# Performance work log

Measured on AMD Instinct MI355X. Metric: run time of the kernel, lower is better.

## Reference

```python
import jax, jax.numpy as jnp
import numpy as np

# Level-7 icosphere: nv vertices, nf faces
NV, NF = 163842, 327680
IN_C, NECK_C, OUT_C, B = 64, 32, 128, 2
EPS = 1e-5


def setup_inputs() -> dict:
    key = jax.random.key(0)
    ks = jax.random.split(key, 16)
    f32 = jnp.float32
    d = {}
    d['x'] = jax.random.normal(ks[0], (B, IN_C, NV), f32)
    # conv1 (1x1), bn1
    d['w1'] = jax.random.normal(ks[1], (NECK_C, IN_C), f32) * 0.05
    d['b1'] = jnp.zeros((NECK_C,), f32)
    d['gamma1'] = jnp.ones((NECK_C,), f32); d['beta1'] = jnp.zeros((NECK_C,), f32)
    # MeshConv: coeffs (out,in,4 taps: id, lap, grad_ew, grad_ns) + bias
    d['coeffs'] = jax.random.normal(ks[2], (NECK_C, NECK_C, 4), f32) * 0.05
    d['mc_bias'] = jnp.zeros((NECK_C,), f32)
    d['gamma2'] = jnp.ones((NECK_C,), f32); d['beta2'] = jnp.zeros((NECK_C,), f32)
    # conv3 (1x1), bn3
    d['w3'] = jax.random.normal(ks[3], (OUT_C, NECK_C), f32) * 0.05
    d['b3'] = jnp.zeros((OUT_C,), f32)
    d['gamma3'] = jnp.ones((OUT_C,), f32); d['beta3'] = jnp.zeros((OUT_C,), f32)
    # shortcut conv_ + bn_ (diff_chan since in!=out)
    d['wsc'] = jax.random.normal(ks[4], (OUT_C, IN_C), f32) * 0.05
    d['bsc'] = jnp.zeros((OUT_C,), f32)
    d['gammasc'] = jnp.ones((OUT_C,), f32); d['betasc'] = jnp.zeros((OUT_C,), f32)
    # sparse mesh operators (gather indices + values):
    # G: face gradient, 3 components per face from 3 face vertices
    d['idx_G'] = jax.random.randint(ks[5], (NF, 3), 0, NV, jnp.int32)
    d['vals_G'] = jax.random.normal(ks[6], (NF, 3, 3), f32) * 0.1
    # EW/NS tangent direction per face (3-vectors)
    d['EW'] = jax.random.normal(ks[7], (NF, 3), f32)
    d['NS'] = jax.random.normal(ks[8], (NF, 3), f32)
    # L: vertex laplacian, ~7 nnz per row
    d['idx_L'] = jax.random.randint(ks[9], (NV, 7), 0, NV, jnp.int32)
    d['vals_L'] = jax.random.normal(ks[10], (NV, 7), f32) * 0.1
    # F2V: face-to-vertex averaging, ~6 faces per vertex
    d['idx_F2V'] = jax.random.randint(ks[11], (NV, 6), 0, NF, jnp.int32)
    d['vals_F2V'] = jax.random.uniform(ks[12], (NV, 6), f32) / 6.0
    return d


def _bn(x, g, b):
    # training-mode BatchNorm1d over (batch, spatial), per channel
    m = x.mean(axis=(0, 2), keepdims=True)
    v = ((x - m) ** 2).mean(axis=(0, 2), keepdims=True)
    return g[None, :, None] * (x - m) * jax.lax.rsqrt(v + EPS) + b[None, :, None]


def _conv1x1(x, w, b):
    return jnp.einsum('oc,bcn->bon', w, x) + b[None, :, None]


def _mesh_conv(x, coeffs, bias, idx_G, vals_G, EW, NS, idx_L, vals_L, idx_F2V, vals_F2V):
    # laplacian: sparse matmul via gather  (B,C,NV)
    lap = jnp.einsum('bcnk,nk->bcn', x[:, :, idx_L], vals_L)
    # face gradient: (B,C,NF,3 components)
    grad_face = jnp.einsum('bcfj,fij->bcfi', x[:, :, idx_G], vals_G)
    g_ew = jnp.einsum('bcfi,fi->bcf', grad_face, EW)
    g_ns = jnp.einsum('bcfi,fi->bcf', grad_face, NS)
    # face -> vertex averaging
    gv_ew = jnp.einsum('bcnk,nk->bcn', g_ew[:, :, idx_F2V], vals_F2V)
    gv_ns = jnp.einsum('bcnk,nk->bcn', g_ns[:, :, idx_F2V], vals_F2V)
    feat = jnp.stack([x, lap, gv_ew, gv_ns], axis=-1)  # (B,C,NV,4)
    return jnp.einsum('bcnk,ock->bon', feat, coeffs) + bias[None, :, None]


def reference(x, w1, b1, gamma1, beta1, coeffs, mc_bias, gamma2, beta2,
              w3, b3, gamma3, beta3, wsc, bsc, gammasc, betasc,
              idx_G, vals_G, EW, NS, idx_L, vals_L, idx_F2V, vals_F2V):
    # shortcut branch (diff_chan)
    x2 = _bn(_conv1x1(x, wsc, bsc), gammasc, betasc)
    # main branch
    h = jax.nn.relu(_bn(_conv1x1(x, w1, b1), gamma1, beta1))
    h = _mesh_conv(h, coeffs, mc_bias, idx_G, vals_G, EW, NS, idx_L, vals_L, idx_F2V, vals_F2V)
    h = jax.nn.relu(_bn(h, gamma2, beta2))
    h = _bn(_conv1x1(h, w3, b3), gamma3, beta3)
    return jax.nn.relu(h + x2)
```

## Files before the change

### kernel.cpp

```cpp
#include <hip/hip_runtime.h>

#define NV   163842
#define NF   327680
#define BB   2
#define INC  64
#define NECK 32
#define OUTC 128
#define NT   (BB*NV)
#define EPSB 1e-5f

typedef unsigned short ushort_t;
typedef __attribute__((ext_vector_type(8))) short bf16x8;
typedef __attribute__((ext_vector_type(4))) float f32x4;

#define F_SX8  0
#define F_SS8  512
#define F_A1   33280
#define F_C1   33312
#define F_ASC  33344
#define F_CSC  33472
#define F_S2S  33600
#define F_S2Q  33632
#define F_A2   33664
#define F_C2   33696
#define F_SHR  33728
#define F_SS2  33760
#define F_A3   34784
#define F_C3   34912
#define F_CF   35040
#define STATN  35168
#define F_W1B  35200
#define F_CFB  36224
#define F_Y1   38272
#define F_H2   (F_Y1 + NT*16)
#define F_I18  (F_H2 + NT*16)
#define F_WEW  (F_I18 + NV*18)
#define F_WNS  (F_WEW + NV*18)
#define F_XB   (F_WNS + NV*18)

#define FSTR 136

__device__ __forceinline__ float bf2f(ushort_t u) {
    union { unsigned int i; float f; } x; x.i = ((unsigned int)u) << 16; return x.f;
}
__device__ __forceinline__ ushort_t f2bf(float f) {
    union { float f; unsigned int i; } x; x.f = f;
    unsigned int r = x.i + 0x7fffu + ((x.i >> 16) & 1u);
    return (ushort_t)(r >> 16);
}

__global__ __launch_bounds__(256) void k_xcvt(const float* __restrict__ x,
                                              float* __restrict__ ws,
                                              ushort_t* __restrict__ xb) {
    __shared__ float SSl[64 * 68 + 64];
    const int tid = threadIdx.x;
    const int w = tid >> 6, l = tid & 63;
    const int o16 = l & 15, kg = l >> 4;

    for (int i = tid; i < 64 * 68 + 64; i += 256) SSl[i] = 0.f;
    __syncthreads();

    f32x4 acc[10];
#pragma unroll
    for (int i = 0; i < 10; ++i) acc[i] = (f32x4){0.f, 0.f, 0.f, 0.f};
    f32x4 accS[4];
#pragma unroll
    for (int i = 0; i < 4; ++i) accS[i] = (f32x4){0.f, 0.f, 0.f, 0.f};

    bf16x8 onesf;
    {
        short ov = (o16 == 0) ? (short)0x3F80 : (short)0;
#pragma unroll
        for (int j = 0; j < 8; ++j) onesf[j] = ov;
    }

    const int NCHB = (NV + 63) >> 6;
    const int NW = gridDim.x * 4;
    for (int cid = blockIdx.x * 4 + w; cid < 2 * NCHB; cid += NW) {
        const int b = (cid >= NCHB) ? 1 : 0;
        const int tc = cid - b * NCHB;
        const int n0 = tc << 6;
        const float* xsrc = x + (size_t)b * 64 * NV;
        const bool full = (n0 + 64 <= NV);
        const int n = n0 + l;
        if (n < NV) {
            unsigned int pk[32];
#pragma unroll
            for (int c2 = 0; c2 < 32; ++c2) {
                float f0 = xsrc[(size_t)(2 * c2) * NV + n];
                float f1 = xsrc[(size_t)(2 * c2 + 1) * NV + n];
                pk[c2] = (unsigned int)f2bf(f0) | ((unsigned int)f2bf(f1) << 16);
            }
            ushort_t* row = xb + (size_t)(b * NV + n) * 64;
#pragma unroll
            for (int j = 0; j < 8; ++j) {
                uint4 q = make_uint4(pk[4 * j], pk[4 * j + 1], pk[4 * j + 2], pk[4 * j + 3]);
                *(uint4*)(row + j * 8) = q;
            }
        }
        bf16x8 fr[4][2];
#pragma unroll
        for (int mt = 0; mt < 4; ++mt) {
            const float* rp = xsrc + (size_t)(mt * 16 + o16) * NV + n0;
#pragma unroll
            for (int ks = 0; ks < 2; ++ks) {
                const int v0 = ks * 32 + kg * 8;
                float f[8];
                if (full) {
                    float4 q0 = *(const float4*)(rp + v0);
                    float4 q1 = *(const float4*)(rp + v0 + 4);
                    f[0] = q0.x; f[1] = q0.y; f[2] = q0.z; f[3] = q0.w;
                    f[4] = q1.x; f[5] = q1.y; f[6] = q1.z; f[7] = q1.w;
                } else {
#pragma unroll
                    for (int j = 0; j < 8; ++j)
                        f[j] = (n0 + v0 + j < NV) ? rp[v0 + j] : 0.f;
                }
                bf16x8 fb;
#pragma unroll
                for (int j = 0; j < 8; ++j) fb[j] = (short)f2bf(f[j]);
                fr[mt][ks] = fb;
            }
        }
#pragma unroll
        for (int ks = 0; ks < 2; ++ks) {
            int tt = 0;
#pragma unroll
            for (int mt = 0; mt < 4; ++mt) {
#pragma unroll
                for (int nt2 = 0; nt2 < 4; ++nt2) {
                    if (nt2 >= mt) {
                        acc[tt] = __builtin_amdgcn_mfma_f32_16x16x32_bf16(fr[mt][ks], fr[nt2][ks], acc[tt], 0, 0, 0);
                        ++tt;
                    }
                }
                accS[mt] = __builtin_amdgcn_mfma_f32_16x16x32_bf16(onesf, fr[mt][ks], accS[mt], 0, 0, 0);
            }
        }
    }
    {
        int tt = 0;
#pragma unroll
        for (int mt = 0; mt < 4; ++mt) {
#pragma unroll
            for (int nt2 = 0; nt2 < 4; ++nt2) {
                if (nt2 >= mt) {
#pragma unroll
                    for (int r = 0; r < 4; ++r) {
                        const int row = mt * 16 + kg * 4 + r;
                        const int col = nt2 * 16 + o16;
                        atomicAdd(&SSl[row * 68 + col], acc[tt][r]);
                    }
                    ++tt;
                }
            }
            if (kg == 0) atomicAdd(&SSl[64 * 68 + mt * 16 + o16], accS[mt][0]);
        }
    }
    __syncthreads();
    {
        float* SSg = ws + F_SS8 + (size_t)(blockIdx.x & 7) * 4096;
        for (int i = tid; i < 64 * 64; i += 256) {
            const int r = i >> 6, c = i & 63;
            if (c >= r) {
                float v = SSl[r * 68 + c];
                if (v != 0.f) atomicAdd(&SSg[r * 64 + c], v);
            }
        }
        if (tid < 64) atomicAdd(&ws[F_SX8 + (blockIdx.x & 7) * 64 + tid], SSl[64 * 68 + tid]);
    }
}

__global__ __launch_bounds__(256) void k_fold1(const float* __restrict__ w1,
                                               const float* __restrict__ g1,
                                               const float* __restrict__ be1,
                                               const float* __restrict__ wsc,
                                               const float* __restrict__ gsc,
                                               const float* __restrict__ besc,
                                               float* __restrict__ ws,
                                               ushort_t* __restrict__ w1b) {
    __shared__ float SSl[4096];
    __shared__ float Sxl[64];
    const int tid = threadIdx.x;
    for (int i = tid; i < 4096; i += 256) {
        const int r = i >> 6, c = i & 63;
        float v = 0.f;
        if (c >= r) {
#pragma unroll
            for (int s = 0; s < 8; ++s) v += ws[F_SS8 + s * 4096 + i];
        }
        SSl[i] = v;
    }
    if (tid < 64) {
        float v = 0.f;
#pragma unroll
        for (int s = 0; s < 8; ++s) v += ws[F_SX8 + s * 64 + tid];
        Sxl[tid] = v;
    }
    __syncthreads();
    for (int i = tid; i < 4096; i += 256) {
        const int r = i >> 6, c = i & 63;
        if (c < r) SSl[i] = SSl[c * 64 + r];
    }
    __syncthreads();
    if (tid >= 32) return;
    const int bk = blockIdx.x;
    const float* w;
    float gamma, beta;
    float *pa, *pc;
    if (bk == 0) {
        w = w1 + tid * 64; gamma = g1[tid]; beta = be1[tid];
        pa = ws + F_A1 + tid; pc = ws + F_C1 + tid;
    } else {
        int o = (bk - 1) * 32 + tid;
        w = wsc + o * 64; gamma = gsc[o]; beta = besc[o];
        pa = ws + F_ASC + o; pc = ws + F_CSC + o;
    }
    float4 wr[16];
#pragma unroll
    for (int i = 0; i < 16; ++i) wr[i] = *(const float4*)(w + i * 4);
    float dotm = 0.f, quad = 0.f;
#pragma unroll
    for (int i4 = 0; i4 < 16; ++i4) {
        float4 wi = wr[i4];
        float rd[4] = {0.f, 0.f, 0.f, 0.f};
#pragma unroll
        for (int j4 = 0; j4 < 16; ++j4) {
            float4 wj = wr[j4];
#pragma unroll
            for (int r = 0; r < 4; ++r) {
                const float* row = &SSl[(i4 * 4 + r) * 64 + j4 * 4];
                rd[r] += row[0] * wj.x + row[1] * wj.y + row[2] * wj.z + row[3] * wj.w;
            }
        }
        dotm += wi.x * Sxl[i4 * 4] + wi.y * Sxl[i4 * 4 + 1] + wi.z * Sxl[i4 * 4 + 2] + wi.w * Sxl[i4 * 4 + 3];
        quad += wi.x * rd[0] + wi.y * rd[1] + wi.z * rd[2] + wi.w * rd[3];
    }
    const float invN = 1.0f / (float)NT;
    const float mean0 = dotm * invN;
    const float var = quad * invN - mean0 * mean0;
    const float a = gamma * rsqrtf(var + EPSB);
    *pa = a;
    *pc = beta - a * mean0;
    if (bk == 0) {
#pragma unroll
        for (int i4 = 0; i4 < 16; ++i4) {
            w1b[tid * 64 + i4 * 4 + 0] = f2bf(a * wr[i4].x);
            w1b[tid * 64 + i4 * 4 + 1] = f2bf(a * wr[i4].y);
            w1b[tid * 64 + i4 * 4 + 2] = f2bf(a * wr[i4].z);
            w1b[tid * 64 + i4 * 4 + 3] = f2bf(a * wr[i4].w);
        }
    }
}

__global__ __launch_bounds__(256) void k_conv1(const ushort_t* __restrict__ xb,
                                               const ushort_t* __restrict__ w1b,
                                               const float* __restrict__ ws,
                                               ushort_t* __restrict__ y1) {
    const int tid = threadIdx.x;
    const int w = tid >> 6, l = tid & 63;
    const int o16 = l & 15, kg = l >> 4;
    bf16x8 af[2][2];
#pragma unroll
    for (int mt = 0; mt < 2; ++mt)
#pragma unroll
        for (int ks = 0; ks < 2; ++ks)
            af[mt][ks] = *(const bf16x8*)(w1b + (mt * 16 + o16) * 64 + ks * 32 + kg * 8);
    float c1r[2][4];
#pragma unroll
    for (int mt = 0; mt < 2; ++mt)
#pragma unroll
        for (int r = 0; r < 4; ++r)
            c1r[mt][r] = ws[F_C1 + mt * 16 + kg * 4 + r];

    const int NCH = (NT + 63) >> 6;
    for (int ch = blockIdx.x * 4 + w; ch < NCH; ch += gridDim.x * 4) {
        const int n0 = ch << 6;
        bf16x8 bf[4][2];
#pragma unroll
        for (int nt = 0; nt < 4; ++nt) {
            int row = n0 + nt * 16 + o16;
            row = row < NT ? row : NT - 1;
#pragma unroll
            for (int ks = 0; ks < 2; ++ks)
                bf[nt][ks] = *(const bf16x8*)(xb + (size_t)row * 64 + ks * 32 + kg * 8);
        }
        f32x4 acc[2][4];
#pragma unroll
        for (int mt = 0; mt < 2; ++mt)
#pragma unroll
            for (int nt = 0; nt < 4; ++nt) acc[mt][nt] = (f32x4){0.f, 0.f, 0.f, 0.f};
#pragma unroll
        for (int mt = 0; mt < 2; ++mt)
#pragma unroll
            for (int nt = 0; nt < 4; ++nt)
#pragma unroll
                for (int ks = 0; ks < 2; ++ks)
                    acc[mt][nt] = __builtin_amdgcn_mfma_f32_16x16x32_bf16(af[mt][ks], bf[nt][ks], acc[mt][nt], 0, 0, 0);
#pragma unroll
        for (int nt = 0; nt < 4; ++nt) {
            const int vert = n0 + nt * 16 + o16;
            if (vert < NT) {
#pragma unroll
                for (int mt = 0; mt < 2; ++mt) {
                    uint2 p;
                    p.x = (unsigned)f2bf(fmaxf(acc[mt][nt][0] + c1r[mt][0], 0.f)) |
                          ((unsigned)f2bf(fmaxf(acc[mt][nt][1] + c1r[mt][1], 0.f)) << 16);
                    p.y = (unsigned)f2bf(fmaxf(acc[mt][nt][2] + c1r[mt][2], 0.f)) |
                          ((unsigned)f2bf(fmaxf(acc[mt][nt][3] + c1r[mt][3], 0.f)) << 16);
                    *(uint2*)(y1 + (size_t)vert * 32 + mt * 16 + kg * 4) = p;
                }
            }
        }
    }
}

__global__ __launch_bounds__(256) void k_w18(const int* __restrict__ idx_F2V,
                                             const float* __restrict__ vals_F2V,
                                             const int* __restrict__ idx_G,
                                             const float* __restrict__ vals_G,
                                             const float* __restrict__ EW,
                                             const float* __restrict__ NS,
                                             int* __restrict__ i18,
                                             float* __restrict__ wew,
                                             float* __restrict__ wns) {
    const int n = blockIdx.x * 256 + threadIdx.x;
    if (n >= NV) return;
#pragma unroll
    for (int k = 0; k < 6; ++k) {
        int f = idx_F2V[n * 6 + k];
        float fv = vals_F2V[n * 6 + k];
        float e0 = EW[f * 3], e1 = EW[f * 3 + 1], e2 = EW[f * 3 + 2];
        float s0 = NS[f * 3], s1 = NS[f * 3 + 1], s2 = NS[f * 3 + 2];
#pragma unroll
        for (int j = 0; j < 3; ++j) {
            float g0 = vals_G[f * 9 + j], g1 = vals_G[f * 9 + 3 + j], g2 = vals_G[f * 9 + 6 + j];
            i18[n * 18 + k * 3 + j] = idx_G[f * 3 + j];
            wew[n * 18 + k * 3 + j] = fv * (g0 * e0 + g1 * e1 + g2 * e2);
            wns[n * 18 + k * 3 + j] = fv * (g0 * s0 + g1 * s1 + g2 * s2);
        }
    }
}

__global__ __launch_bounds__(256) void k_cvtcoef(const float* __restrict__ c,
                                                 ushort_t* __restrict__ cb) {
    int i = blockIdx.x * 256 + threadIdx.x;
    if (i < 4096) cb[i] = f2bf(c[i]);
}

__global__ __launch_bounds__(256, 4) void k_meshconv(const ushort_t* __restrict__ y1,
                                                     const ushort_t* __restrict__ cfb,
                                                     const int* __restrict__ idx_L,
                                                     const float* __restrict__ vals_L,
                                                     const int* __restrict__ i18,
                                                     const float* __restrict__ w18ew,
                                                     const float* __restrict__ w18ns,
                                                     ushort_t* __restrict__ h2,
                                                     float* __restrict__ ws) {
    __shared__ __align__(16) ushort_t feat[4][32 * FSTR];
    __shared__ float sred[64];
    const int tid = threadIdx.x;
    const int w = __builtin_amdgcn_readfirstlane(tid >> 6);
    const int lane = tid & 63;
    ushort_t* fw = &feat[w][0];
    const int v4 = lane >> 4;
    const int c2 = lane & 15;
    const int o16 = lane & 15;
    const int kg = lane >> 4;

    if (tid < 64) sred[tid] = 0.f;
    __syncthreads();

    float ssum[8], sssq[8];
#pragma unroll
    for (int i = 0; i < 8; ++i) { ssum[i] = 0.f; sssq[i] = 0.f; }

    const int gw = blockIdx.x * 4 + w;
    const int NW = gridDim.x * 4;
    const int NCHB = (NV + 31) >> 5;

    for (int cid = gw; cid < 2 * NCHB; cid += NW) {
        const int b = (cid >= NCHB) ? 1 : 0;
        const int vch = cid - b * NCHB;
        const int n0 = vch << 5;
        const ushort_t* yb = y1 + (size_t)b * (NV * 32);
        for (int jj = 0; jj < 8; ++jj) {
            const int n = n0 + jj * 4 + v4;
            const bool ok = (n < NV);
            const int nn = ok ? n : NV - 1;
            unsigned int qs = *(const unsigned int*)(yb + (nn << 5) + (c2 << 1));
            float fx0 = bf2f((ushort_t)(qs & 0xffffu));
            float fx1 = bf2f((ushort_t)(qs >> 16));
            float lap0 = 0.f, lap1 = 0.f, ge0 = 0.f, ge1 = 0.f, gn0 = 0.f, gn1 = 0.f;
            const int* ilp = idx_L + nn * 7;
            const float* vlp = vals_L + nn * 7;
#pragma unroll
            for (int j = 0; j < 7; ++j) {
                const int vi = ilp[j];
                const float wv = vlp[j];
                unsigned int q = *(const unsigned int*)(yb + (vi << 5) + (c2 << 1));
                lap0 += wv * bf2f((ushort_t)(q & 0xffffu));
                lap1 += wv * bf2f((ushort_t)(q >> 16));
            }
            const int* igp = i18 + nn * 18;
            const float* wep = w18ew + nn * 18;
            const float* wnp = w18ns + nn * 18;
#pragma unroll
            for (int j = 0; j < 18; ++j) {
                const int vi = igp[j];
                const float we = wep[j], wn = wnp[j];
                unsigned int q = *(const unsigned int*)(yb + (vi << 5) + (c2 << 1));
                float v0 = bf2f((ushort_t)(q & 0xffffu));
                float v1 = bf2f((ushort_t)(q >> 16));
                ge0 += we * v0; ge1 += we * v1;
                gn0 += wn * v0; gn1 += wn * v1;
            }
            unsigned int u0 = 0u, u1 = 0u, u2 = 0u, u3 = 0u;
            if (ok) {
                u0 = (unsigned int)f2bf(fx0) | ((unsigned int)f2bf(lap0) << 16);
                u1 = (unsigned int)f2bf(ge0) | ((unsigned int)f2bf(gn0) << 16);
                u2 = (unsigned int)f2bf(fx1) | ((unsigned int)f2bf(lap1) << 16);
                u3 = (unsigned int)f2bf(ge1) | ((unsigned int)f2bf(gn1) << 16);
            }
            const int inst = jj * 4 + v4;
            *(uint4*)(fw + inst * FSTR + (c2 << 3)) = make_uint4(u0, u1, u2, u3);
        }
        f32x4 acc[2][2];
#pragma unroll
        for (int mt = 0; mt < 2; ++mt)
#pragma unroll
            for (int nt = 0; nt < 2; ++nt) acc[mt][nt] = (f32x4){0.f, 0.f, 0.f, 0.f};
        bf16x8 bfr[2][4];
#pragma unroll
        for (int nt = 0; nt < 2; ++nt)
#pragma unroll
            for (int kt = 0; kt < 4; ++kt)
                bfr[nt][kt] = *(const bf16x8*)(fw + (nt * 16 + o16) * FSTR + kt * 32 + kg * 8);
#pragma unroll
        for (int mt = 0; mt < 2; ++mt) {
#pragma unroll
            for (int kt = 0; kt < 4; ++kt) {
                bf16x8 af = *(const bf16x8*)(cfb + (mt * 16 + o16) * 128 + kt * 32 + kg * 8);
                acc[mt][0] = __builtin_amdgcn_mfma_f32_16x16x32_bf16(af, bfr[0][kt], acc[mt][0], 0, 0, 0);
                acc[mt][1] = __builtin_amdgcn_mfma_f32_16x16x32_bf16(af, bfr[1][kt], acc[mt][1], 0, 0, 0);
            }
        }
#pragma unroll
        for (int nt = 0; nt < 2; ++nt) {
            const int vert = n0 + nt * 16 + o16;
            if (vert < NV) {
                const int rowb = ((b * NV + vert) << 5);
#pragma unroll
                for (int mt = 0; mt < 2; ++mt) {
#pragma unroll
                    for (int r = 0; r < 4; ++r) {
                        float v = acc[mt][nt][r];
                        int o = mt * 16 + kg * 4 + r;
                        h2[rowb + o] = f2bf(v);
                        ssum[mt * 4 + r] += v;
                        sssq[mt * 4 + r] += v * v;
                    }
                }
            }
        }
    }

#pragma unroll
    for (int si = 0; si < 8; ++si) {
#pragma unroll
        for (int m = 1; m < 16; m <<= 1) {
            ssum[si] += __shfl_xor(ssum[si], m, 16);
            sssq[si] += __shfl_xor(sssq[si], m, 16);
        }
    }
    if (o16 == 0) {
#pragma unroll
        for (int mt = 0; mt < 2; ++mt)
#pragma unroll
            for (int r = 0; r < 4; ++r) {
                int o = mt * 16 + kg * 4 + r;
                atomicAdd(&sred[o], ssum[mt * 4 + r]);
                atomicAdd(&sred[32 + o], sssq[mt * 4 + r]);
            }
    }
    __syncthreads();
    if (tid < 64) atomicAdd(&ws[F_S2S + tid], sred[tid]);
}

__global__ void k_fold2(const float* __restrict__ g2, const float* __restrict__ be2,
                        float* __restrict__ ws) {
    const int c = threadIdx.x;
    if (c < 32) {
        const float invN = 1.0f / (float)NT;
        float m = ws[F_S2S + c] * invN;
        float var = ws[F_S2Q + c] * invN - m * m;
        float a = g2[c] * rsqrtf(var + EPSB);
        ws[F_A2 + c] = a;
        ws[F_C2 + c] = be2[c] - a * m;
    }
}

__global__ __launch_bounds__(256) void k_hrmoments(const ushort_t* __restrict__ h2,
                                                   float* __restrict__ ws) {
    __shared__ __align__(16) ushort_t tile[4][32 * 40];
    __shared__ float red[1056];
    const int tid = threadIdx.x;
    const int w = tid >> 6, l = tid & 63;
    ushort_t* T = &tile[w][0];
    const int c8 = (l & 3) * 8;
    const int v0 = l >> 2;
    const int fr = l & 15, kg = l >> 4;

    for (int i = tid; i < 1056; i += 256) red[i] = 0.f;
    __syncthreads();

    float a2r[8], c2r[8];
#pragma unroll
    for (int j = 0; j < 8; ++j) { a2r[j] = ws[F_A2 + c8 + j]; c2r[j] = ws[F_C2 + c8 + j]; }

    f32x4 acc[2][2];
#pragma unroll
    for (int a = 0; a < 2; ++a)
#pragma unroll
        for (int b = 0; b < 2; ++b) acc[a][b] = (f32x4){0.f, 0.f, 0.f, 0.f};
    float ssum[8];
#pragma unroll
    for (int j = 0; j < 8; ++j) ssum[j] = 0.f;

    const int NCH = (NT + 31) >> 5;
    for (int ch = blockIdx.x * 4 + w; ch < NCH; ch += gridDim.x * 4) {
        const int s0 = ch << 5;
#pragma unroll
        for (int i = 0; i < 2; ++i) {
            const int vert = i * 16 + v0;
            const int s = s0 + vert;
            uint4 q = make_uint4(0u, 0u, 0u, 0u);
            const bool ok = (s < NT);
            if (ok) q = *(const uint4*)(h2 + (size_t)s * 32 + c8);
            const ushort_t* qs = (const ushort_t*)&q;
            ushort_t hb[8];
#pragma unroll
            for (int j = 0; j < 8; ++j) {
                float hv = ok ? fmaxf(a2r[j] * bf2f(qs[j]) + c2r[j], 0.f) : 0.f;
                ssum[j] += hv;
                hb[j] = f2bf(hv);
            }
#pragma unroll
            for (int j = 0; j < 8; ++j) T[(c8 + j) * 40 + vert] = hb[j];
        }
        bf16x8 f0 = *(const bf16x8*)(T + fr * 40 + kg * 8);
        bf16x8 f1 = *(const bf16x8*)(T + (16 + fr) * 40 + kg * 8);
        acc[0][0] = __builtin_amdgcn_mfma_f32_16x16x32_bf16(f0, f0, acc[0][0], 0, 0, 0);
        acc[0][1] = __builtin_amdgcn_mfma_f32_16x16x32_bf16(f0, f1, acc[0][1], 0, 0, 0);
        acc[1][0] = __builtin_amdgcn_mfma_f32_16x16x32_bf16(f1, f0, acc[1][0], 0, 0, 0);
        acc[1][1] = __builtin_amdgcn_mfma_f32_16x16x32_bf16(f1, f1, acc[1][1], 0, 0, 0);
    }
#pragma unroll
    for (int mt = 0; mt < 2; ++mt)
#pragma unroll
        for (int nt = 0; nt < 2; ++nt)
#pragma unroll
            for (int r = 0; r < 4; ++r)
                atomicAdd(&red[(mt * 16 + kg * 4 + r) * 32 + nt * 16 + fr], acc[mt][nt][r]);
#pragma unroll
    for (int j = 0; j < 8; ++j) {
        float s = ssum[j];
        s += __shfl_xor(s, 4); s += __shfl_xor(s, 8);
        s += __shfl_xor(s, 16); s += __shfl_xor(s, 32);
        if (v0 == 0) atomicAdd(&red[1024 + c8 + j], s);
    }
    __syncthreads();
    for (int i = tid; i < 1024; i += 256) atomicAdd(&ws[F_SS2 + i], red[i]);
    if (tid < 32) atomicAdd(&ws[F_SHR + tid], red[1024 + tid]);
}

__global__ __launch_bounds__(128) void k_fold3(const float* __restrict__ w3,
                                               const float* __restrict__ wsc,
                                               const float* __restrict__ g3,
                                               const float* __restrict__ be3,
                                               float* __restrict__ ws,
                                               ushort_t* __restrict__ wfb) {
    __shared__ float SSl[1024];
    __shared__ float Sl[32];
    const int tid = threadIdx.x;
    for (int i = tid; i < 1024; i += 128) SSl[i] = ws[F_SS2 + i];
    if (tid < 32) Sl[tid] = ws[F_SHR + tid];
    __syncthreads();
    const int o = tid;
    float4 wr[8];
#pragma unroll
    for (int i = 0; i < 8; ++i) wr[i] = *(const float4*)(w3 + o * 32 + i * 4);
    float dotm = 0.f, quad = 0.f;
#pragma unroll
    for (int i4 = 0; i4 < 8; ++i4) {
        float4 wi = wr[i4];
        float rd[4] = {0.f, 0.f, 0.f, 0.f};
#pragma unroll
        for (int j4 = 0; j4 < 8; ++j4) {
            float4 wj = wr[j4];
#pragma unroll
            for (int r = 0; r < 4; ++r) {
                const float* row = &SSl[(i4 * 4 + r) * 32 + j4 * 4];
                rd[r] += row[0] * wj.x + row[1] * wj.y + row[2] * wj.z + row[3] * wj.w;
            }
        }
        dotm += wi.x * Sl[i4 * 4] + wi.y * Sl[i4 * 4 + 1] + wi.z * Sl[i4 * 4 + 2] + wi.w * Sl[i4 * 4 + 3];
        quad += wi.x * rd[0] + wi.y * rd[1] + wi.z * rd[2] + wi.w * rd[3];
    }
    const float invN = 1.0f / (float)NT;
    const float mean0 = dotm * invN;
    const float var = quad * invN - mean0 * mean0;
    const float a = g3[o] * rsqrtf(var + EPSB);
    const float cbias = be3[o] - a * mean0;
    ws[F_A3 + o] = a;
    ws[F_C3 + o] = cbias;
    const float asc = ws[F_ASC + o], csc = ws[F_CSC + o];
    ws[F_CF + o] = cbias + csc;
#pragma unroll
    for (int i4 = 0; i4 < 8; ++i4) {
        wfb[o * 96 + i4 * 4 + 0] = f2bf(a * wr[i4].x);
        wfb[o * 96 + i4 * 4 + 1] = f2bf(a * wr[i4].y);
        wfb[o * 96 + i4 * 4 + 2] = f2bf(a * wr[i4].z);
        wfb[o * 96 + i4 * 4 + 3] = f2bf(a * wr[i4].w);
    }
    for (int j = 0; j < 64; ++j)
        wfb[o * 96 + 32 + j] = f2bf(asc * wsc[o * 64 + j]);
}

__global__ __launch_bounds__(256) void k_final(const ushort_t* __restrict__ xb,
                                               const ushort_t* __restrict__ h2,
                                               const ushort_t* __restrict__ wfb,
                                               const float* __restrict__ ws,
                                               float* __restrict__ out) {
    __shared__ __align__(16) ushort_t feat[32 * 104];
    const int tid = threadIdx.x;
    const int w = tid >> 6, l = tid & 63;
    const int fr = l & 15, kg = l >> 4;

    bf16x8 af[2][3];
#pragma unroll
    for (int mt = 0; mt < 2; ++mt)
#pragma unroll
        for (int kt = 0; kt < 3; ++kt)
            af[mt][kt] = *(const bf16x8*)(wfb + (w * 32 + mt * 16 + fr) * 96 + kt * 32 + kg * 8);
    float cfr[2][4];
#pragma unroll
    for (int mt = 0; mt < 2; ++mt)
#pragma unroll
        for (int r = 0; r < 4; ++r)
            cfr[mt][r] = ws[F_CF + w * 32 + mt * 16 + kg * 4 + r];

    const int hv = tid >> 3, hc4 = (tid & 7) * 4;
    float a2r[4], c2r[4];
#pragma unroll
    for (int j = 0; j < 4; ++j) { a2r[j] = ws[F_A2 + hc4 + j]; c2r[j] = ws[F_C2 + hc4 + j]; }
    const int xv = tid >> 3, xseg = tid & 7;

    const int NCHK = (NV + 31) >> 5;
    for (int cid = blockIdx.x; cid < 2 * NCHK; cid += gridDim.x) {
        const int b = (cid >= NCHK) ? 1 : 0;
        const int t = cid - b * NCHK;
        const int n0 = t << 5;
        const int rem = NV - n0 < 32 ? NV - n0 : 32;
        {
            const int s = b * NV + n0 + hv;
            const bool ok = (hv < rem);
            uint2 q = make_uint2(0u, 0u);
            if (ok) q = *(const uint2*)(h2 + (size_t)s * 32 + hc4);
            const ushort_t* qs = (const ushort_t*)&q;
            unsigned int p0 = 0u, p1 = 0u;
            if (ok) {
                float h0 = fmaxf(a2r[0] * bf2f(qs[0]) + c2r[0], 0.f);
                float h1 = fmaxf(a2r[1] * bf2f(qs[1]) + c2r[1], 0.f);
                float h2v = fmaxf(a2r[2] * bf2f(qs[2]) + c2r[2], 0.f);
                float h3 = fmaxf(a2r[3] * bf2f(qs[3]) + c2r[3], 0.f);
                p0 = (unsigned int)f2bf(h0) | ((unsigned int)f2bf(h1) << 16);
                p1 = (unsigned int)f2bf(h2v) | ((unsigned int)f2bf(h3) << 16);
            }
            *(uint2*)(feat + hv * 104 + hc4) = make_uint2(p0, p1);
        }
        {
            const int s = b * NV + n0 + xv;
            uint4 q = make_uint4(0u, 0u, 0u, 0u);
            if (xv < rem) q = *(const uint4*)(xb + (size_t)s * 64 + xseg * 8);
            *(uint4*)(feat + xv * 104 + 32 + xseg * 8) = q;
        }
        __syncthreads();
        bf16x8 bf[2][3];
#pragma unroll
        for (int nt = 0; nt < 2; ++nt)
#pragma unroll
            for (int kt = 0; kt < 3; ++kt)
                bf[nt][kt] = *(const bf16x8*)(feat + (nt * 16 + fr) * 104 + kt * 32 + kg * 8);
        __syncthreads();
        f32x4 acc[2][2];
#pragma unroll
        for (int mt = 0; mt < 2; ++mt)
#pragma unroll
            for (int nt = 0; nt < 2; ++nt) acc[mt][nt] = (f32x4){0.f, 0.f, 0.f, 0.f};
#pragma unroll
        for (int mt = 0; mt < 2; ++mt)
#pragma unroll
            for (int nt = 0; nt < 2; ++nt)
#pragma unroll
                for (int kt = 0; kt < 3; ++kt)
                    acc[mt][nt] = __builtin_amdgcn_mfma_f32_16x16x32_bf16(af[mt][kt], bf[nt][kt], acc[mt][nt], 0, 0, 0);
#pragma unroll
        for (int mt = 0; mt < 2; ++mt) {
#pragma unroll
            for (int nt = 0; nt < 2; ++nt) {
                const int col = n0 + nt * 16 + fr;
                if (col < NV) {
                    float* po = out + (size_t)(b * 128 + w * 32 + mt * 16 + kg * 4) * NV + col;
#pragma unroll
                    for (int r = 0; r < 4; ++r)
                        po[(size_t)r * NV] = fmaxf(acc[mt][nt][r] + cfr[mt][r], 0.f);
                }
            }
        }
    }
}

extern "C" void kernel_launch(void* const* d_in, const int* in_sizes, int n_in,
                              void* d_out, int out_size, void* d_ws, size_t ws_size,
                              hipStream_t stream) {
    (void)in_sizes; (void)n_in; (void)out_size; (void)ws_size;
    const float* x        = (const float*)d_in[0];
    const float* w1       = (const float*)d_in[1];
    const float* g1       = (const float*)d_in[3];
    const float* be1      = (const float*)d_in[4];
    const float* coeffs   = (const float*)d_in[5];
    const float* g2       = (const float*)d_in[7];
    const float* be2      = (const float*)d_in[8];
    const float* w3       = (const float*)d_in[9];
    const float* g3       = (const float*)d_in[11];
    const float* be3      = (const float*)d_in[12];
    const float* wsc      = (const float*)d_in[13];
    const float* gsc      = (const float*)d_in[15];
    const float* besc     = (const float*)d_in[16];
    const int*   idx_G    = (const int*)d_in[17];
    const float* vals_G   = (const float*)d_in[18];
    const float* EW       = (const float*)d_in[19];
    const float* NS       = (const float*)d_in[20];
    const int*   idx_L    = (const int*)d_in[21];
    const float* vals_L   = (const float*)d_in[22];
    const int*   idx_F2V  = (const int*)d_in[23];
    const float* vals_F2V = (const float*)d_in[24];
    float* ws  = (float*)d_ws;
    float* out = (float*)d_out;

    ushort_t* w1b = (ushort_t*)(ws + F_W1B);
    ushort_t* cfb = (ushort_t*)(ws + F_CFB);
    ushort_t* y1  = (ushort_t*)(ws + F_Y1);
    ushort_t* h2  = (ushort_t*)(ws + F_H2);
    ushort_t* xb  = (ushort_t*)(ws + F_XB);
    ushort_t* wfb = (ushort_t*)(ws + F_Y1);

    hipMemsetAsync(ws, 0, STATN * sizeof(float), stream);
    hipLaunchKernelGGL(k_xcvt, dim3(1280), dim3(256), 0, stream, x, ws, xb);
    hipLaunchKernelGGL(k_w18, dim3((NV + 255) / 256), dim3(256), 0, stream,
                       idx_F2V, vals_F2V, idx_G, vals_G, EW, NS,
                       (int*)(ws + F_I18), ws + F_WEW, ws + F_WNS);
    hipLaunchKernelGGL(k_cvtcoef, dim3(16), dim3(256), 0, stream, coeffs, cfb);
    hipLaunchKernelGGL(k_fold1, dim3(5), dim3(256), 0, stream, w1, g1, be1, wsc, gsc, besc, ws, w1b);
    hipLaunchKernelGGL(k_conv1, dim3(1280), dim3(256), 0, stream, xb, w1b, ws, y1);
    hipLaunchKernelGGL(k_meshconv, dim3(1024), dim3(256), 0, stream,
                       y1, cfb, idx_L, vals_L,
                       (const int*)(ws + F_I18), ws + F_WEW, ws + F_WNS,
                       h2, ws);
    hipLaunchKernelGGL(k_fold2, dim3(1), dim3(32), 0, stream, g2, be2, ws);
    hipLaunchKernelGGL(k_hrmoments, dim3(1024), dim3(256), 0, stream, h2, ws);
    hipLaunchKernelGGL(k_fold3, dim3(1), dim3(128), 0, stream, w3, wsc, g3, be3, ws, wfb);
    hipLaunchKernelGGL(k_final, dim3(2048), dim3(256), 0, stream, xb, h2, wfb, ws, out);
}
```

Baseline: 544.3 us.

## Fuse conv1 into x conversion, defer BN1 affine+ReLU into meshconv gathers

Computes the raw conv1 product (unscaled bf16 w1) inside k_xcvt from an LDS-staged transposed tile, so the separate k_conv1 pass that re-read xb disappears. BN1 scale, shift and ReLU are applied on the fly at every gather inside k_meshconv. The w18 precompute and the coefficient and w1 conversions are merged into one prep kernel, and fold2 moves into k_hrmoments, cutting the launch count. Meshconv also now processes both batches in one chunk. The costs are extra per-gather FMAs, a large LDS allocation in k_xcvt that may lower occupancy, and y1 stored before normalisation, which changes where bf16 rounding happens.

```diff
diff --git a/kernel.cpp b/kernel.cpp
--- a/kernel.cpp
+++ b/kernel.cpp
@@ -49,16 +49,61 @@
     return (ushort_t)(r >> 16);
 }
 
-__global__ __launch_bounds__(256) void k_xcvt(const float* __restrict__ x,
-                                              float* __restrict__ ws,
-                                              ushort_t* __restrict__ xb) {
+__global__ __launch_bounds__(256) void k_prep(const int* __restrict__ idx_F2V,
+                                              const float* __restrict__ vals_F2V,
+                                              const int* __restrict__ idx_G,
+                                              const float* __restrict__ vals_G,
+                                              const float* __restrict__ EW,
+                                              const float* __restrict__ NS,
+                                              const float* __restrict__ coeffs,
+                                              const float* __restrict__ w1,
+                                              int* __restrict__ i18,
+                                              float* __restrict__ wew,
+                                              float* __restrict__ wns,
+                                              ushort_t* __restrict__ cfb,
+                                              ushort_t* __restrict__ w1b) {
+    const int gid = blockIdx.x * 256 + threadIdx.x;
+    if (gid < 4096) cfb[gid] = f2bf(coeffs[gid]);
+    if (gid < 2048) w1b[gid] = f2bf(w1[gid]);
+    const int n = gid;
+    if (n >= NV) return;
+#pragma unroll
+    for (int k = 0; k < 6; ++k) {
+        int f = idx_F2V[n * 6 + k];
+        float fv = vals_F2V[n * 6 + k];
+        float e0 = EW[f * 3], e1 = EW[f * 3 + 1], e2 = EW[f * 3 + 2];
+        float s0 = NS[f * 3], s1 = NS[f * 3 + 1], s2 = NS[f * 3 + 2];
+#pragma unroll
+        for (int j = 0; j < 3; ++j) {
+            float g0 = vals_G[f * 9 + j], g1 = vals_G[f * 9 + 3 + j], g2 = vals_G[f * 9 + 6 + j];
+            i18[n * 18 + k * 3 + j] = idx_G[f * 3 + j];
+            wew[n * 18 + k * 3 + j] = fv * (g0 * e0 + g1 * e1 + g2 * e2);
+            wns[n * 18 + k * 3 + j] = fv * (g0 * s0 + g1 * s1 + g2 * s2);
+        }
+    }
+}
+
+__global__ __launch_bounds__(256, 3) void k_xcvt(const float* __restrict__ x,
+                                                 const ushort_t* __restrict__ w1b,
+                                                 float* __restrict__ ws,
+                                                 ushort_t* __restrict__ xb,
+                                                 ushort_t* __restrict__ y1) {
+    __shared__ __align__(16) ushort_t TB[4][64 * 68];
     __shared__ float SSl[64 * 68 + 64];
     const int tid = threadIdx.x;
     const int w = tid >> 6, l = tid & 63;
     const int o16 = l & 15, kg = l >> 4;
+    ushort_t* TBw = &TB[w][0];
 
     for (int i = tid; i < 64 * 68 + 64; i += 256) SSl[i] = 0.f;
     __syncthreads();
+
+    bf16x8 aw[2][2];
+#pragma unroll
+    for (int mt = 0; mt < 2; ++mt)
+#pragma unroll
+        for (int ks = 0; ks < 2; ++ks)
+            aw[mt][ks] = *(const bf16x8*)(w1b + (mt * 16 + o16) * 64 + ks * 32 + kg * 8);
 
     f32x4 acc[10];
 #pragma unroll
@@ -82,20 +127,61 @@
         const int n0 = tc << 6;
         const float* xsrc = x + (size_t)b * 64 * NV;
         const bool full = (n0 + 64 <= NV);
-        const int n = n0 + l;
-        if (n < NV) {
-            unsigned int pk[32];
-#pragma unroll
-            for (int c2 = 0; c2 < 32; ++c2) {
-                float f0 = xsrc[(size_t)(2 * c2) * NV + n];
-                float f1 = xsrc[(size_t)(2 * c2 + 1) * NV + n];
-                pk[c2] = (unsigned int)f2bf(f0) | ((unsigned int)f2bf(f1) << 16);
-            }
-            ushort_t* row = xb + (size_t)(b * NV + n) * 64;
-#pragma unroll
-            for (int j = 0; j < 8; ++j) {
-                uint4 q = make_uint4(pk[4 * j], pk[4 * j + 1], pk[4 * j + 2], pk[4 * j + 3]);
-                *(uint4*)(row + j * 8) = q;
+        {
+            const int n = n0 + l;
+            ushort_t* trow = TBw + l * 68;
+            if (n < NV) {
+                unsigned int pk[32];
+#pragma unroll
+                for (int c2 = 0; c2 < 32; ++c2) {
+                    float f0 = xsrc[(size_t)(2 * c2) * NV + n];
+                    float f1 = xsrc[(size_t)(2 * c2 + 1) * NV + n];
+                    pk[c2] = (unsigned int)f2bf(f0) | ((unsigned int)f2bf(f1) << 16);
+                }
+                ushort_t* row = xb + (size_t)(b * NV + n) * 64;
+#pragma unroll
+                for (int j = 0; j < 8; ++j) {
+                    uint4 q = make_uint4(pk[4 * j], pk[4 * j + 1], pk[4 * j + 2], pk[4 * j + 3]);
+                    *(uint4*)(row + j * 8) = q;
+                    *(uint4*)(trow + j * 8) = q;
+                }
+            } else {
+                uint4 z = make_uint4(0u, 0u, 0u, 0u);
+#pragma unroll
+                for (int j = 0; j < 8; ++j) *(uint4*)(trow + j * 8) = z;
+            }
+        }
+        {
+            bf16x8 bfc[4][2];
+#pragma unroll
+            for (int nt = 0; nt < 4; ++nt)
+#pragma unroll
+                for (int ks = 0; ks < 2; ++ks)
+                    bfc[nt][ks] = *(const bf16x8*)(TBw + (nt * 16 + o16) * 68 + ks * 32 + kg * 8);
+            f32x4 ac1[2][4];
+#pragma unroll
+            for (int mt = 0; mt < 2; ++mt)
+#pragma unroll
+                for (int nt = 0; nt < 4; ++nt) ac1[mt][nt] = (f32x4){0.f, 0.f, 0.f, 0.f};
+#pragma unroll
+            for (int mt = 0; mt < 2; ++mt)
+#pragma unroll
+                for (int nt = 0; nt < 4; ++nt)
+#pragma unroll
+                    for (int ks = 0; ks < 2; ++ks)
+                        ac1[mt][nt] = __builtin_amdgcn_mfma_f32_16x16x32_bf16(aw[mt][ks], bfc[nt][ks], ac1[mt][nt], 0, 0, 0);
+#pragma unroll
+            for (int nt = 0; nt < 4; ++nt) {
+                const int vert = n0 + nt * 16 + o16;
+                if (vert < NV) {
+#pragma unroll
+                    for (int mt = 0; mt < 2; ++mt) {
+                        uint2 p;
+                        p.x = (unsigned)f2bf(ac1[mt][nt][0]) | ((unsigned)f2bf(ac1[mt][nt][1]) << 16);
+                        p.y = (unsigned)f2bf(ac1[mt][nt][2]) | ((unsigned)f2bf(ac1[mt][nt][3]) << 16);
+                        *(uint2*)(y1 + ((size_t)b * NV + vert) * 32 + mt * 16 + kg * 4) = p;
+                    }
+                }
             }
         }
         bf16x8 fr[4][2];
@@ -146,11 +232,8 @@
             for (int nt2 = 0; nt2 < 4; ++nt2) {
                 if (nt2 >= mt) {
 #pragma unroll
-                    for (int r = 0; r < 4; ++r) {
-                        const int row = mt * 16 + kg * 4 + r;
-                        const int col = nt2 * 16 + o16;
-                        atomicAdd(&SSl[row * 68 + col], acc[tt][r]);
-                    }
+                    for (int r = 0; r < 4; ++r)
+                        atomicAdd(&SSl[(mt * 16 + kg * 4 + r) * 68 + nt2 * 16 + o16], acc[tt][r]);
                     ++tt;
                 }
             }
@@ -177,8 +260,7 @@
                                                const float* __restrict__ wsc,
                                                const float* __restrict__ gsc,
                                                const float* __restrict__ besc,
-                                               float* __restrict__ ws,
-                                               ushort_t* __restrict__ w1b) {
+                                               float* __restrict__ ws) {
     __shared__ float SSl[4096];
     __shared__ float Sxl[64];
     const int tid = threadIdx.x;
@@ -242,110 +324,6 @@
     const float a = gamma * rsqrtf(var + EPSB);
     *pa = a;
     *pc = beta - a * mean0;
-    if (bk == 0) {
-#pragma unroll
-        for (int i4 = 0; i4 < 16; ++i4) {
-            w1b[tid * 64 + i4 * 4 + 0] = f2bf(a * wr[i4].x);
-            w1b[tid * 64 + i4 * 4 + 1] = f2bf(a * wr[i4].y);
-            w1b[tid * 64 + i4 * 4 + 2] = f2bf(a * wr[i4].z);
-            w1b[tid * 64 + i4 * 4 + 3] = f2bf(a * wr[i4].w);
-        }
-    }
-}
-
-__global__ __launch_bounds__(256) void k_conv1(const ushort_t* __restrict__ xb,
-                                               const ushort_t* __restrict__ w1b,
-                                               const float* __restrict__ ws,
-                                               ushort_t* __restrict__ y1) {
-    const int tid = threadIdx.x;
-    const int w = tid >> 6, l = tid & 63;
-    const int o16 = l & 15, kg = l >> 4;
-    bf16x8 af[2][2];
-#pragma unroll
-    for (int mt = 0; mt < 2; ++mt)
-#pragma unroll
-        for (int ks = 0; ks < 2; ++ks)
-            af[mt][ks] = *(const bf16x8*)(w1b + (mt * 16 + o16) * 64 + ks * 32 + kg * 8);
-    float c1r[2][4];
-#pragma unroll
-    for (int mt = 0; mt < 2; ++mt)
-#pragma unroll
-        for (int r = 0; r < 4; ++r)
-            c1r[mt][r] = ws[F_C1 + mt * 16 + kg * 4 + r];
-
-    const int NCH = (NT + 63) >> 6;
-    for (int ch = blockIdx.x * 4 + w; ch < NCH; ch += gridDim.x * 4) {
-        const int n0 = ch << 6;
-        bf16x8 bf[4][2];
-#pragma unroll
-        for (int nt = 0; nt < 4; ++nt) {
-            int row = n0 + nt * 16 + o16;
-            row = row < NT ? row : NT - 1;
-#pragma unroll
-            for (int ks = 0; ks < 2; ++ks)
-                bf[nt][ks] = *(const bf16x8*)(xb + (size_t)row * 64 + ks * 32 + kg * 8);
-        }
-        f32x4 acc[2][4];
-#pragma unroll
-        for (int mt = 0; mt < 2; ++mt)
-#pragma unroll
-            for (int nt = 0; nt < 4; ++nt) acc[mt][nt] = (f32x4){0.f, 0.f, 0.f, 0.f};
-#pragma unroll
-        for (int mt = 0; mt < 2; ++mt)
-#pragma unroll
-            for (int nt = 0; nt < 4; ++nt)
-#pragma unroll
-                for (int ks = 0; ks < 2; ++ks)
-                    acc[mt][nt] = __builtin_amdgcn_mfma_f32_16x16x32_bf16(af[mt][ks], bf[nt][ks], acc[mt][nt], 0, 0, 0);
-#pragma unroll
-        for (int nt = 0; nt < 4; ++nt) {
-            const int vert = n0 + nt * 16 + o16;
-            if (vert < NT) {
-#pragma unroll
-                for (int mt = 0; mt < 2; ++mt) {
-                    uint2 p;
-                    p.x = (unsigned)f2bf(fmaxf(acc[mt][nt][0] + c1r[mt][0], 0.f)) |
-                          ((unsigned)f2bf(fmaxf(acc[mt][nt][1] + c1r[mt][1], 0.f)) << 16);
-                    p.y = (unsigned)f2bf(fmaxf(acc[mt][nt][2] + c1r[mt][2], 0.f)) |
-                          ((unsigned)f2bf(fmaxf(acc[mt][nt][3] + c1r[mt][3], 0.f)) << 16);
-                    *(uint2*)(y1 + (size_t)vert * 32 + mt * 16 + kg * 4) = p;
-                }
-            }
-        }
-    }
-}
-
-__global__ __launch_bounds__(256) void k_w18(const int* __restrict__ idx_F2V,
-                                             const float* __restrict__ vals_F2V,
-                                             const int* __restrict__ idx_G,
-                                             const float* __restrict__ vals_G,
-                                             const float* __restrict__ EW,
-                                             const float* __restrict__ NS,
-                                             int* __restrict__ i18,
-                                             float* __restrict__ wew,
-                                             float* __restrict__ wns) {
-    const int n = blockIdx.x * 256 + threadIdx.x;
-    if (n >= NV) return;
-#pragma unroll
-    for (int k = 0; k < 6; ++k) {
-        int f = idx_F2V[n * 6 + k];
-        float fv = vals_F2V[n * 6 + k];
-        float e0 = EW[f * 3], e1 = EW[f * 3 + 1], e2 = EW[f * 3 + 2];
-        float s0 = NS[f * 3], s1 = NS[f * 3 + 1], s2 = NS[f * 3 + 2];
-#pragma unroll
-        for (int j = 0; j < 3; ++j) {
-            float g0 = vals_G[f * 9 + j], g1 = vals_G[f * 9 + 3 + j], g2 = vals_G[f * 9 + 6 + j];
-            i18[n * 18 + k * 3 + j] = idx_G[f * 3 + j];
-            wew[n * 18 + k * 3 + j] = fv * (g0 * e0 + g1 * e1 + g2 * e2);
-            wns[n * 18 + k * 3 + j] = fv * (g0 * s0 + g1 * s1 + g2 * s2);
-        }
-    }
-}
-
-__global__ __launch_bounds__(256) void k_cvtcoef(const float* __restrict__ c,
-                                                 ushort_t* __restrict__ cb) {
-    int i = blockIdx.x * 256 + threadIdx.x;
-    if (i < 4096) cb[i] = f2bf(c[i]);
 }
 
 __global__ __launch_bounds__(256, 4) void k_meshconv(const ushort_t* __restrict__ y1,
@@ -363,11 +341,15 @@
     const int w = __builtin_amdgcn_readfirstlane(tid >> 6);
     const int lane = tid & 63;
     ushort_t* fw = &feat[w][0];
-    const int v4 = lane >> 4;
+    const int gh = lane >> 5;
+    const int bh = (lane >> 4) & 1;
     const int c2 = lane & 15;
     const int o16 = lane & 15;
     const int kg = lane >> 4;
 
+    const float a1_0 = ws[F_A1 + 2 * c2], a1_1 = ws[F_A1 + 2 * c2 + 1];
+    const float c1_0 = ws[F_C1 + 2 * c2], c1_1 = ws[F_C1 + 2 * c2 + 1];
+
     if (tid < 64) sred[tid] = 0.f;
     __syncthreads();
 
@@ -377,20 +359,18 @@
 
     const int gw = blockIdx.x * 4 + w;
     const int NW = gridDim.x * 4;
-    const int NCHB = (NV + 31) >> 5;
-
-    for (int cid = gw; cid < 2 * NCHB; cid += NW) {
-        const int b = (cid >= NCHB) ? 1 : 0;
-        const int vch = cid - b * NCHB;
-        const int n0 = vch << 5;
-        const ushort_t* yb = y1 + (size_t)b * (NV * 32);
+    const int NCH = (NV + 15) >> 4;
+
+    for (int ch = gw; ch < NCH; ch += NW) {
+        const int n0 = ch << 4;
+        const ushort_t* yb = y1 + (size_t)bh * (NV * 32);
         for (int jj = 0; jj < 8; ++jj) {
-            const int n = n0 + jj * 4 + v4;
+            const int n = n0 + jj * 2 + gh;
             const bool ok = (n < NV);
             const int nn = ok ? n : NV - 1;
             unsigned int qs = *(const unsigned int*)(yb + (nn << 5) + (c2 << 1));
-            float fx0 = bf2f((ushort_t)(qs & 0xffffu));
-            float fx1 = bf2f((ushort_t)(qs >> 16));
+            float fx0 = fmaxf(fmaf(a1_0, bf2f((ushort_t)(qs & 0xffffu)), c1_0), 0.f);
+            float fx1 = fmaxf(fmaf(a1_1, bf2f((ushort_t)(qs >> 16)), c1_1), 0.f);
             float lap0 = 0.f, lap1 = 0.f, ge0 = 0.f, ge1 = 0.f, gn0 = 0.f, gn1 = 0.f;
             const int* ilp = idx_L + nn * 7;
             const float* vlp = vals_L + nn * 7;
@@ -399,8 +379,10 @@
                 const int vi = ilp[j];
                 const float wv = vlp[j];
                 unsigned int q = *(const unsigned int*)(yb + (vi << 5) + (c2 << 1));
-                lap0 += wv * bf2f((ushort_t)(q & 0xffffu));
-                lap1 += wv * bf2f((ushort_t)(q >> 16));
+                float v0 = fmaxf(fmaf(a1_0, bf2f((ushort_t)(q & 0xffffu)), c1_0), 0.f);
+                float v1 = fmaxf(fmaf(a1_1, bf2f((ushort_t)(q >> 16)), c1_1), 0.f);
+                lap0 += wv * v0;
+                lap1 += wv * v1;
             }
             const int* igp = i18 + nn * 18;
             const float* wep = w18ew + nn * 18;
@@ -410,8 +392,8 @@
                 const int vi = igp[j];
                 const float we = wep[j], wn = wnp[j];
                 unsigned int q = *(const unsigned int*)(yb + (vi << 5) + (c2 << 1));
-                float v0 = bf2f((ushort_t)(q & 0xffffu));
-                float v1 = bf2f((ushort_t)(q >> 16));
+                float v0 = fmaxf(fmaf(a1_0, bf2f((ushort_t)(q & 0xffffu)), c1_0), 0.f);
+                float v1 = fmaxf(fmaf(a1_1, bf2f((ushort_t)(q >> 16)), c1_1), 0.f);
                 ge0 += we * v0; ge1 += we * v1;
                 gn0 += wn * v0; gn1 += wn * v1;
             }
@@ -422,7 +404,7 @@
                 u2 = (unsigned int)f2bf(fx1) | ((unsigned int)f2bf(lap1) << 16);
                 u3 = (unsigned int)f2bf(ge1) | ((unsigned int)f2bf(gn1) << 16);
             }
-            const int inst = jj * 4 + v4;
+            const int inst = bh * 16 + jj * 2 + gh;
             *(uint4*)(fw + inst * FSTR + (c2 << 3)) = make_uint4(u0, u1, u2, u3);
         }
         f32x4 acc[2][2];
@@ -445,11 +427,11 @@
                 acc[mt][1] = __builtin_amdgcn_mfma_f32_16x16x32_bf16(af, bfr[1][kt], acc[mt][1], 0, 0, 0);
             }
         }
-#pragma unroll
-        for (int nt = 0; nt < 2; ++nt) {
-            const int vert = n0 + nt * 16 + o16;
-            if (vert < NV) {
-                const int rowb = ((b * NV + vert) << 5);
+        const int n = n0 + o16;
+        if (n < NV) {
+#pragma unroll
+            for (int nt = 0; nt < 2; ++nt) {
+                const int rowb = ((nt * NV + n) << 5);
 #pragma unroll
                 for (int mt = 0; mt < 2; ++mt) {
 #pragma unroll
@@ -487,23 +469,13 @@
     if (tid < 64) atomicAdd(&ws[F_S2S + tid], sred[tid]);
 }
 
-__global__ void k_fold2(const float* __restrict__ g2, const float* __restrict__ be2,
-                        float* __restrict__ ws) {
-    const int c = threadIdx.x;
-    if (c < 32) {
-        const float invN = 1.0f / (float)NT;
-        float m = ws[F_S2S + c] * invN;
-        float var = ws[F_S2Q + c] * invN - m * m;
-        float a = g2[c] * rsqrtf(var + EPSB);
-        ws[F_A2 + c] = a;
-        ws[F_C2 + c] = be2[c] - a * m;
-    }
-}
-
 __global__ __launch_bounds__(256) void k_hrmoments(const ushort_t* __restrict__ h2,
+                                                   const float* __restrict__ g2,
+                                                   const float* __restrict__ be2,
                                                    float* __restrict__ ws) {
     __shared__ __align__(16) ushort_t tile[4][32 * 40];
     __shared__ float red[1056];
+    __shared__ float sA2[32], sC2[32];
     const int tid = threadIdx.x;
     const int w = tid >> 6, l = tid & 63;
     ushort_t* T = &tile[w][0];
@@ -511,12 +483,21 @@
     const int v0 = l >> 2;
     const int fr = l & 15, kg = l >> 4;
 
+    if (tid < 32) {
+        const float invN = 1.0f / (float)NT;
+        float m = ws[F_S2S + tid] * invN;
+        float var = ws[F_S2Q + tid] * invN - m * m;
+        float a = g2[tid] * rsqrtf(var + EPSB);
+        float c = be2[tid] - a * m;
+        sA2[tid] = a; sC2[tid] = c;
+        ws[F_A2 + tid] = a; ws[F_C2 + tid] = c;
+    }
     for (int i = tid; i < 1056; i += 256) red[i] = 0.f;
     __syncthreads();
 
     float a2r[8], c2r[8];
 #pragma unroll
-    for (int j = 0; j < 8; ++j) { a2r[j] = ws[F_A2 + c8 + j]; c2r[j] = ws[F_C2 + c8 + j]; }
+    for (int j = 0; j < 8; ++j) { a2r[j] = sA2[c8 + j]; c2r[j] = sC2[c8 + j]; }
 
     f32x4 acc[2][2];
 #pragma unroll
@@ -757,19 +738,16 @@
     ushort_t* wfb = (ushort_t*)(ws + F_Y1);
 
     hipMemsetAsync(ws, 0, STATN * sizeof(float), stream);
-    hipLaunchKernelGGL(k_xcvt, dim3(1280), dim3(256), 0, stream, x, ws, xb);
-    hipLaunchKernelGGL(k_w18, dim3((NV + 255) / 256), dim3(256), 0, stream,
-                       idx_F2V, vals_F2V, idx_G, vals_G, EW, NS,
-                       (int*)(ws + F_I18), ws + F_WEW, ws + F_WNS);
-    hipLaunchKernelGGL(k_cvtcoef, dim3(16), dim3(256), 0, stream, coeffs, cfb);
-    hipLaunchKernelGGL(k_fold1, dim3(5), dim3(256), 0, stream, w1, g1, be1, wsc, gsc, besc, ws, w1b);
-    hipLaunchKernelGGL(k_conv1, dim3(1280), dim3(256), 0, stream, xb, w1b, ws, y1);
+    hipLaunchKernelGGL(k_prep, dim3((NV + 255) / 256), dim3(256), 0, stream,
+                       idx_F2V, vals_F2V, idx_G, vals_G, EW, NS, coeffs, w1,
+                       (int*)(ws + F_I18), ws + F_WEW, ws + F_WNS, cfb, w1b);
+    hipLaunchKernelGGL(k_xcvt, dim3(1280), dim3(256), 0, stream, x, w1b, ws, xb, y1);
+    hipLaunchKernelGGL(k_fold1, dim3(5), dim3(256), 0, stream, w1, g1, be1, wsc, gsc, besc, ws);
     hipLaunchKernelGGL(k_meshconv, dim3(1024), dim3(256), 0, stream,
                        y1, cfb, idx_L, vals_L,
                        (const int*)(ws + F_I18), ws + F_WEW, ws + F_WNS,
                        h2, ws);
-    hipLaunchKernelGGL(k_fold2, dim3(1), dim3(32), 0, stream, g2, be2, ws);
-    hipLaunchKernelGGL(k_hrmoments, dim3(1024), dim3(256), 0, stream, h2, ws);
+    hipLaunchKernelGGL(k_hrmoments, dim3(1024), dim3(256), 0, stream, h2, g2, be2, ws);
     hipLaunchKernelGGL(k_fold3, dim3(1), dim3(128), 0, stream, w3, wsc, g3, be3, ws, wfb);
     hipLaunchKernelGGL(k_final, dim3(2048), dim3(256), 0, stream, xb, h2, wfb, ws, out);
 }
```

Measured after the change: 718.7 us. 1.32x slower.
